# Performance work log

Hardware: AMD Instinct MI355X
Metric: run time of the kernel (lower is better)

Reference implementation:

```python
import jax, jax.numpy as jnp
import numpy as np

NUM_HEADS = 16
KEY_DIM = 64
VALUE_DIM = 64
UPDATE_STEPS_MAX = 3  # loop runs UPDATE_STEPS_MAX+1 attention evaluations, eps=0 so no early exit
LN_EPS = 1e-5


def _layernorm(x, gamma, beta):
    mu = jnp.mean(x, axis=-1, keepdims=True)
    var = jnp.var(x, axis=-1, keepdims=True)
    return (x - mu) * jax.lax.rsqrt(var + LN_EPS) * gamma + beta


def setup_inputs() -> dict:
    key = jax.random.key(0)
    ks = jax.random.split(key, 16)
    B, S, D = 2, 2048, 1024
    Hd = NUM_HEADS * KEY_DIM
    Vd = NUM_HEADS * VALUE_DIM
    s = 1.0 / np.sqrt(D)
    return {
        'query': jax.random.normal(ks[0], (B, S, D), jnp.float32),
        'key':   jax.random.normal(ks[1], (B, S, D), jnp.float32),
        'value': jax.random.normal(ks[2], (B, S, D), jnp.float32),
        'Wq': jax.random.normal(ks[3], (D, Hd), jnp.float32) * s,
        'bq': jnp.zeros((Hd,), jnp.float32),
        'Wk': jax.random.normal(ks[4], (D, Hd), jnp.float32) * s,
        'bk': jnp.zeros((Hd,), jnp.float32),
        'Wv': jax.random.normal(ks[5], (D, Vd), jnp.float32) * s,
        'bv': jnp.zeros((Vd,), jnp.float32),
        'Wo': jax.random.normal(ks[6], (Vd, D), jnp.float32) * s,
        'bo': jnp.zeros((D,), jnp.float32),
        'gamma': jnp.ones((KEY_DIM,), jnp.float32),
        'beta':  jnp.zeros((KEY_DIM,), jnp.float32),
    }


def reference(query, key, value, Wq, bq, Wk, bk, Wv, bv, Wo, bo, gamma, beta):
    B, Sq, D = query.shape
    Sk = key.shape[1]
    # projections -> (B, H, S, d)
    q = (query @ Wq + bq).reshape(B, Sq, NUM_HEADS, KEY_DIM).transpose(0, 2, 1, 3)
    k = (key   @ Wk + bk).reshape(B, Sk, NUM_HEADS, KEY_DIM).transpose(0, 2, 1, 3)
    v = (value @ Wv + bv).reshape(B, Sk, NUM_HEADS, VALUE_DIM).transpose(0, 2, 1, 3)
    # pattern normalization (applied once before the Hopfield loop)
    q = _layernorm(q, gamma, beta)
    k = _layernorm(k, gamma, beta)
    scale = jnp.sqrt(jnp.asarray(KEY_DIM, q.dtype))
    # Hopfield iterations: UPDATE_STEPS_MAX query refinements + final readout
    for i in range(UPDATE_STEPS_MAX + 1):
        scores = jnp.einsum('bhqd,bhkd->bhqk', q, k) / scale
        attn = jax.nn.softmax(scores, axis=-1)
        if i < UPDATE_STEPS_MAX:
            q = jnp.einsum('bhqk,bhkd->bhqd', attn, k)
    out = jnp.einsum('bhqk,bhkd->bhqd', attn, v)  # (B,H,Sq,VALUE_DIM)
    out = out.transpose(0, 2, 1, 3).reshape(B, Sq, NUM_HEADS * VALUE_DIM)
    return out @ Wo + bo
```

## Files before the change

### kernel.cpp

```cpp
#include <hip/hip_runtime.h>

typedef unsigned short u16;
typedef __attribute__((ext_vector_type(8))) short bf16x8;
typedef __attribute__((ext_vector_type(4))) short bf16x4;
typedef __attribute__((ext_vector_type(4))) float f32x4;
typedef __attribute__((ext_vector_type(4))) u16 u16x4;

#define C1 0.18033688011112042f
#define NEGM (-64.0f*C1)

#define GLDS(g, l) __builtin_amdgcn_global_load_lds( \
    (const __attribute__((address_space(1))) void*)(g), \
    (__attribute__((address_space(3))) void*)(l), 16, 0, 0)

__device__ __forceinline__ float fastexp2(float x){
  float r;
  asm("v_exp_f32 %0, %1" : "=v"(r) : "v"(x));
  return r;
}

__device__ __forceinline__ unsigned cvtpk(float x0, float x1){
  unsigned r;
  asm("v_cvt_pk_bf16_f32 %0, %1, %2" : "=v"(r) : "v"(x0), "v"(x1));
  return r;
}

__device__ __forceinline__ bf16x4 pk4(float x0, float x1, float x2, float x3){
  union { unsigned u[2]; bf16x4 b; } o;
  o.u[0] = cvtpk(x0, x1);
  o.u[1] = cvtpk(x2, x3);
  return o.b;
}

__device__ __forceinline__ u16 f2bf(float x){
  unsigned u = __float_as_uint(x);
  u += 0x7fffu + ((u >> 16) & 1u);
  return (u16)(u >> 16);
}
__device__ __forceinline__ float bf2f(u16 h){ return __uint_as_float(((unsigned)h) << 16); }
__device__ __forceinline__ void fsplit(float x, u16 &h, u16 &l){
  h = f2bf(x);
  l = f2bf(x - bf2f(h));
}

__device__ __forceinline__ int swz(int slot, int r){
  return slot ^ (r & 7);
}

__device__ __forceinline__ bf16x8 frag(const bf16x8* lds, int r, int slot){
  return lds[r*8 + swz(slot, r)];
}

__device__ __forceinline__ bf16x4 frag64(const bf16x8* lds, int r, int slot, int half){
  return ((const bf16x4*)&lds[r*8 + swz(slot, r)])[half ^ ((r >> 3) & 1)];
}

template<int ROWS>
__device__ __forceinline__ void stage_glds(bf16x8* lds, const u16* __restrict__ g,
                                           size_t row0, int ldg, int col0, int tid, int w){
#pragma unroll
  for (int p = 0; p < ROWS/32; ++p){
    int idx = p*256 + tid;
    int r = idx >> 3, slot = idx & 7;
    int ss = swz(slot, r);
    GLDS(g + (row0 + (size_t)r)*(size_t)ldg + col0 + ss*8, &lds[p*256 + (w<<6)]);
  }
}

__device__ __forceinline__ f32x4 mfma3(bf16x8 xh, bf16x8 xl, bf16x8 yh, bf16x8 yl, f32x4 c){
  c = __builtin_amdgcn_mfma_f32_16x16x32_bf16(xh, yh, c, 0, 0, 0);
  c = __builtin_amdgcn_mfma_f32_16x16x32_bf16(xh, yl, c, 0, 0, 0);
  c = __builtin_amdgcn_mfma_f32_16x16x32_bf16(xl, yh, c, 0, 0, 0);
  return c;
}

__device__ __forceinline__ void exchange_hi(const f32x4* X, int srcA, int srcB, bool sel_hi,
                                            bf16x8& oh0, bf16x8& oh1)
{
  unsigned hi[8];
#pragma unroll
  for (int a = 0; a < 4; ++a)
#pragma unroll
    for (int b0 = 0; b0 < 2; ++b0)
      hi[a*2+b0] = cvtpk(X[a][2*b0], X[a][2*b0+1]);
  unsigned OH[8];
#pragma unroll
  for (int f = 0; f < 8; ++f){
    const int t0 = (f>>2)*4 + (f&1);
    const int sl = ((f&3)>>1) ? srcB : srcA;
    unsigned h0 = (unsigned)__shfl((int)hi[t0],     sl, 64);
    unsigned h2 = (unsigned)__shfl((int)hi[t0 + 2], sl, 64);
    OH[f] = sel_hi ? h2 : h0;
  }
  union U { unsigned u[4]; bf16x8 b; };
  U a0, a1;
#pragma unroll
  for (int c = 0; c < 4; ++c){ a0.u[c]=OH[c]; a1.u[c]=OH[4+c]; }
  oh0=a0.b; oh1=a1.b;
}

__global__ void __launch_bounds__(256) k_split3(
    const float* __restrict__ xq, const float* __restrict__ xk, const float* __restrict__ xv,
    u16* __restrict__ qh, u16* __restrict__ kh, u16* __restrict__ vh, int n4){
  const int which = blockIdx.y;
  const float* x = which == 0 ? xq : which == 1 ? xk : xv;
  u16* hh = which == 0 ? qh : which == 1 ? kh : vh;
  for (int i = blockIdx.x*256 + threadIdx.x; i < n4; i += gridDim.x*256){
    float4 v = ((const float4*)x)[i];
    u16x4 h;
    h[0] = f2bf(v.x); h[1] = f2bf(v.y); h[2] = f2bf(v.z); h[3] = f2bf(v.w);
    *(u16x4*)(hh + (size_t)i*4) = h;
  }
}

__global__ void __launch_bounds__(256) k_wsplit4(
    const float* __restrict__ W0, const float* __restrict__ W1,
    const float* __restrict__ W2, const float* __restrict__ W3,
    u16* __restrict__ T0h, u16* __restrict__ T1h, u16* __restrict__ T2h,
    u16* __restrict__ T3h, u16* __restrict__ T3l){
  const int which = blockIdx.z;
  const float* W = which == 0 ? W0 : which == 1 ? W1 : which == 2 ? W2 : W3;
  u16* Th = which == 0 ? T0h : which == 1 ? T1h : which == 2 ? T2h : T3h;
  __shared__ float t[32][33];
  int tx = threadIdx.x & 31, ty = threadIdx.x >> 5;
  int n0 = blockIdx.x*32, k0 = blockIdx.y*32;
#pragma unroll
  for (int i = 0; i < 4; ++i)
    t[ty + 8*i][tx] = W[(size_t)(k0 + ty + 8*i)*1024 + n0 + tx];
  __syncthreads();
#pragma unroll
  for (int i = 0; i < 4; ++i){
    int n = n0 + ty + 8*i, k = k0 + tx;
    if (which == 3){
      u16 a, b; fsplit(t[tx][ty + 8*i], a, b);
      Th[(size_t)n*1024 + k] = a;
      T3l[(size_t)n*1024 + k] = b;
    } else {
      Th[(size_t)n*1024 + k] = f2bf(t[tx][ty + 8*i]);
    }
  }
}

template<int MODE, bool SPLIT>
__global__ void __launch_bounds__(256, 3) k_proj(
    const u16* __restrict__ Ah, const u16* __restrict__ Al,
    const u16* __restrict__ Bh, const u16* __restrict__ Bl,
    const float* __restrict__ bias, const float* __restrict__ gamma, const float* __restrict__ beta,
    u16* __restrict__ Nh,
    u16* __restrict__ Th,
    float* __restrict__ Fo)
{
  __shared__ bf16x8 sAh[128*8], sBh[64*8];
  __shared__ bf16x8 sAl[SPLIT ? 128*8 : 1], sBl[SPLIT ? 64*8 : 1];
  const int tid = threadIdx.x, lane = tid & 63, w = tid >> 6;
  const int cl = lane & 15, gq = lane >> 4;
  const int nt = blockIdx.x, mt = blockIdx.y;
  f32x4 acc[2][4] = {};
  for (int kt = 0; kt < 16; ++kt){
    __syncthreads();
    stage_glds<128>(sAh, Ah, (size_t)mt*128, 1024, kt*64, tid, w);
    stage_glds<64>(sBh, Bh, (size_t)nt*64, 1024, kt*64, tid, w);
    if constexpr (SPLIT){
      stage_glds<128>(sAl, Al, (size_t)mt*128, 1024, kt*64, tid, w);
      stage_glds<64>(sBl, Bl, (size_t)nt*64, 1024, kt*64, tid, w);
    }
    __syncthreads();
#pragma unroll
    for (int ks = 0; ks < 2; ++ks){
      const int slot = ks*4 + gq;
      bf16x8 ah0 = frag(sAh, w*32 + cl, slot);
      bf16x8 ah1 = frag(sAh, w*32 + 16 + cl, slot);
      if constexpr (SPLIT){
        bf16x8 al0 = frag(sAl, w*32 + cl, slot);
        bf16x8 al1 = frag(sAl, w*32 + 16 + cl, slot);
#pragma unroll
        for (int f = 0; f < 4; ++f){
          bf16x8 bh_ = frag(sBh, f*16 + cl, slot);
          bf16x8 bl_ = frag(sBl, f*16 + cl, slot);
          acc[0][f] = mfma3(ah0, al0, bh_, bl_, acc[0][f]);
          acc[1][f] = mfma3(ah1, al1, bh_, bl_, acc[1][f]);
        }
      } else {
#pragma unroll
        for (int f = 0; f < 4; ++f){
          bf16x8 bh_ = frag(sBh, f*16 + cl, slot);
          acc[0][f] = __builtin_amdgcn_mfma_f32_16x16x32_bf16(ah0, bh_, acc[0][f], 0, 0, 0);
          acc[1][f] = __builtin_amdgcn_mfma_f32_16x16x32_bf16(ah1, bh_, acc[1][f], 0, 0, 0);
        }
      }
    }
  }
  float bv[4];
#pragma unroll
  for (int f = 0; f < 4; ++f) bv[f] = bias[nt*64 + f*16 + cl];
  float gm[4], bt[4];
  if constexpr (MODE <= 1){
#pragma unroll
    for (int f = 0; f < 4; ++f){ gm[f] = gamma[f*16 + cl]; bt[f] = beta[f*16 + cl]; }
  }
#pragma unroll
  for (int mi = 0; mi < 2; ++mi){
    float v[4][4];
#pragma unroll
    for (int f = 0; f < 4; ++f)
#pragma unroll
      for (int r = 0; r < 4; ++r) v[f][r] = acc[mi][f][r] + bv[f];
    if constexpr (MODE <= 1){
#pragma unroll
      for (int r = 0; r < 4; ++r){
        float s1 = v[0][r] + v[1][r] + v[2][r] + v[3][r];
        float s2 = v[0][r]*v[0][r] + v[1][r]*v[1][r] + v[2][r]*v[2][r] + v[3][r]*v[3][r];
#pragma unroll
        for (int d = 1; d < 16; d <<= 1){ s1 += __shfl_xor(s1, d); s2 += __shfl_xor(s2, d); }
        float mu = s1 * (1.f/64.f);
        float var = s2 * (1.f/64.f) - mu*mu;
        float rs = rsqrtf(var + 1e-5f);
#pragma unroll
        for (int f = 0; f < 4; ++f) v[f][r] = (v[f][r] - mu)*rs*gm[f] + bt[f];
      }
    }
    const int mrow = mt*128 + w*32 + mi*16 + gq*4;
    if constexpr (MODE == 3){
#pragma unroll
      for (int f = 0; f < 4; ++f)
#pragma unroll
        for (int r = 0; r < 4; ++r)
          Fo[(size_t)(mrow + r)*1024 + nt*64 + f*16 + cl] = v[f][r];
    } else {
      const int b = mrow >> 11, srow = mrow & 2047;
      const size_t hb = (size_t)(b*16 + nt);
      if constexpr (MODE <= 1){
#pragma unroll
        for (int f = 0; f < 4; ++f)
#pragma unroll
          for (int r = 0; r < 4; ++r)
            Nh[(hb*2048 + srow + r)*64 + f*16 + cl] = f2bf(v[f][r]);
      }
      if constexpr (MODE == 1 || MODE == 2){
        const int srow_sw = srow ^ (((cl >> 3) & 1) << 2);
#pragma unroll
        for (int f = 0; f < 4; ++f){
          u16x4 h4;
#pragma unroll
          for (int r = 0; r < 4; ++r) h4[r] = f2bf(v[f][r]);
          *(u16x4*)(Th + (hb*64 + f*16 + cl)*2048 + srow_sw) = h4;
        }
      }
    }
  }
}

__global__ void __launch_bounds__(512, 4) k_hopfield(
    const u16* __restrict__ Qh,
    const u16* __restrict__ Kh,
    const u16* __restrict__ Kth,
    const u16* __restrict__ Vth,
    u16* __restrict__ Oh, u16* __restrict__ Ol)
{
  __shared__ bf16x8 sKh[2][512], sTh[2][512];
  const int tid = threadIdx.x, lane = tid & 63, w = tid >> 6;
  const int cl = lane & 15, gq = lane >> 4;
  int flat = blockIdx.x;
  flat = (flat & 7)*64 + (flat >> 3);
  const int bh = flat >> 4, qt = flat & 15;
  const size_t base = (size_t)bh * (2048*64);
  const int q = qt*128 + w*16 + cl;

  const int sr = tid >> 3, ss = swz(tid & 7, sr);
  const size_t offK = base + (size_t)sr*64 + ss*8;
  const size_t offT = base + (size_t)sr*2048 + ss*8;
  const int wslot = w << 6;

  bf16x8 qfh[2];
#pragma unroll
  for (int ks = 0; ks < 2; ++ks)
    qfh[ks] = *(const bf16x8*)(Qh + base + (size_t)q*64 + ks*32 + gq*8);

  const int srcA = cl + ((gq & 1) << 5);
  const int srcB = srcA + 16;
  const bool sel_hi = gq >= 2;

  const bf16x4 ones = {(short)0x3F80, (short)0x3F80, (short)0x3F80, (short)0x3F80};
  f32x4 accL = {0,0,0,0};
  f32x4 accO[4] = {};

  GLDS(Kh  + offK, &sKh[0][wslot]);
  GLDS(Kth + offT, &sTh[0][wslot]);
  __syncthreads();

#pragma unroll 2
  for (int t = 0; t < 128; ++t){
    const int cur = t & 1, kt = t & 31;
    if (t < 127){
      const int nt_ = t + 1, nb = nt_ & 1, nit = nt_ >> 5, nkt = nt_ & 31;
      const u16* th = (nit < 3) ? Kth : Vth;
      GLDS(Kh + offK + (size_t)nkt*4096, &sKh[nb][wslot]);
      GLDS(th + offT + (size_t)nkt*64,   &sTh[nb][wslot]);
    }
    f32x4 S[4] = {};
    __builtin_amdgcn_s_setprio(1);
#pragma unroll
    for (int ks = 0; ks < 2; ++ks){
      const int slot = ks*4 + gq;
#pragma unroll
      for (int i = 0; i < 4; ++i){
        bf16x8 kh_ = frag(&sKh[cur][0], i*16 + cl, slot);
        S[i] = __builtin_amdgcn_mfma_f32_16x16x32_bf16(kh_, qfh[ks], S[i], 0, 0, 0);
      }
    }
    __builtin_amdgcn_s_setprio(0);
#pragma unroll
    for (int i = 0; i < 4; ++i)
#pragma unroll
      for (int r = 0; r < 4; ++r)
        S[i][r] = fastexp2(__builtin_fmaf(S[i][r], C1, NEGM));
    bf16x4 pf[4];
#pragma unroll
    for (int a = 0; a < 4; ++a)
      pf[a] = pk4(S[a][0], S[a][1], S[a][2], S[a][3]);
    __builtin_amdgcn_s_setprio(1);
#pragma unroll
    for (int a = 0; a < 4; ++a)
      accL = __builtin_amdgcn_mfma_f32_16x16x16bf16_1k(ones, pf[a], accL, 0, 0, 0);
#pragma unroll
    for (int db = 0; db < 4; ++db)
#pragma unroll
      for (int a = 0; a < 4; ++a){
        bf16x4 vh_ = frag64(&sTh[cur][0], db*16 + cl, 2*a + (gq>>1), gq&1);
        accO[db] = __builtin_amdgcn_mfma_f32_16x16x16bf16_1k(vh_, pf[a], accO[db], 0, 0, 0);
      }
    __builtin_amdgcn_s_setprio(0);
    if (kt == 31){
      const float inv = 1.f / accL[0];
      f32x4 vals[4];
#pragma unroll
      for (int db = 0; db < 4; ++db)
#pragma unroll
        for (int r = 0; r < 4; ++r) vals[db][r] = accO[db][r]*inv;
      if (t < 127){
        exchange_hi(vals, srcA, srcB, sel_hi, qfh[0], qfh[1]);
        accL = f32x4{0,0,0,0};
#pragma unroll
        for (int db = 0; db < 4; ++db) accO[db] = f32x4{0,0,0,0};
      } else {
        const int b = bh >> 4, h = bh & 15;
        const size_t row = (size_t)b*2048 + q;
#pragma unroll
        for (int db = 0; db < 4; ++db){
          u16x4 h4, l4;
#pragma unroll
          for (int r = 0; r < 4; ++r){ u16 a_, b_; fsplit(vals[db][r], a_, b_); h4[r] = a_; l4[r] = b_; }
          size_t ix = row*1024 + h*64 + db*16 + gq*4;
          *(u16x4*)(Oh + ix) = h4;
          *(u16x4*)(Ol + ix) = l4;
        }
      }
    }
    __syncthreads();
  }
}

extern "C" void kernel_launch(void* const* d_in, const int* in_sizes, int n_in,
                              void* d_out, int out_size, void* d_ws, size_t ws_size,
                              hipStream_t stream) {
  (void)in_sizes; (void)n_in; (void)out_size; (void)ws_size;
  const float* query = (const float*)d_in[0];
  const float* key   = (const float*)d_in[1];
  const float* value = (const float*)d_in[2];
  const float* Wq = (const float*)d_in[3];
  const float* bq = (const float*)d_in[4];
  const float* Wk = (const float*)d_in[5];
  const float* bk = (const float*)d_in[6];
  const float* Wv = (const float*)d_in[7];
  const float* bv = (const float*)d_in[8];
  const float* Wo = (const float*)d_in[9];
  const float* bo = (const float*)d_in[10];
  const float* gamma = (const float*)d_in[11];
  const float* beta  = (const float*)d_in[12];
  float* out = (float*)d_out;

  char* ws = (char*)d_ws;
  const size_t MB = 1024*1024;
  u16* inq_h = (u16*)(ws + 0*MB),  *inq_l = (u16*)(ws + 8*MB);
  u16* ink_h = (u16*)(ws + 16*MB);
  u16* inv_h = (u16*)(ws + 32*MB);
  u16* wq_h = (u16*)(ws + 48*MB);
  u16* wk_h = (u16*)(ws + 52*MB);
  u16* wv_h = (u16*)(ws + 56*MB);
  u16* wo_h = (u16*)(ws + 60*MB), *wo_l = (u16*)(ws + 62*MB);
  u16* Qh  = (u16*)(ws + 64*MB);
  u16* Kh  = (u16*)(ws + 80*MB);
  u16* Kth = (u16*)(ws + 96*MB);
  u16* Vth = (u16*)(ws + 112*MB);
  u16* Oh = inq_h, *Ol = inq_l;

  const int n4 = 4096*1024/4;
  k_split3<<<dim3(1024, 3), dim3(256), 0, stream>>>(query, key, value,
                                                    inq_h, ink_h, inv_h, n4);
  k_wsplit4<<<dim3(32,32,4), dim3(256), 0, stream>>>(Wq, Wk, Wv, Wo,
                                                     wq_h, wk_h, wv_h, wo_h, wo_l);

  k_proj<0,false><<<dim3(16,32), dim3(256), 0, stream>>>(inq_h, nullptr, wq_h, nullptr, bq, gamma, beta,
                                                         Qh, nullptr, nullptr);
  k_proj<1,false><<<dim3(16,32), dim3(256), 0, stream>>>(ink_h, nullptr, wk_h, nullptr, bk, gamma, beta,
                                                         Kh, Kth, nullptr);
  k_proj<2,false><<<dim3(16,32), dim3(256), 0, stream>>>(inv_h, nullptr, wv_h, nullptr, bv, nullptr, nullptr,
                                                         nullptr, Vth, nullptr);

  k_hopfield<<<dim3(512), dim3(512), 0, stream>>>(Qh, Kh, Kth, Vth, Oh, Ol);

  k_proj<3,true><<<dim3(16,32), dim3(256), 0, stream>>>(Oh, Ol, wo_h, wo_l, bo, nullptr, nullptr,
                                                        nullptr, nullptr, out);
}
```

Measured before the change: 281.1 us.

## Process two query groups per wave in Hopfield kernel to reuse K/V fragments

The Hopfield attention kernel drops from 512 to 256 threads per block, and each wave now handles 32 queries as two 16-row groups instead of 16. Each K and V fragment read from LDS feeds two MFMAs, which halves LDS fragment traffic per MFMA. Each thread issues two async global-to-LDS loads per tile to fill the same buffers. Register pressure roughly doubles for the accumulators and occupancy falls (launch bounds 256,2), which may expose latency.

After: 286.9 us. 1.02x slower.

```diff
diff --git a/kernel.cpp b/kernel.cpp
--- a/kernel.cpp
+++ b/kernel.cpp
@@ -250,7 +250,7 @@
   }
 }
 
-__global__ void __launch_bounds__(512, 4) k_hopfield(
+__global__ void __launch_bounds__(256, 2) k_hopfield(
     const u16* __restrict__ Qh,
     const u16* __restrict__ Kh,
     const u16* __restrict__ Kth,
@@ -264,28 +264,33 @@
   flat = (flat & 7)*64 + (flat >> 3);
   const int bh = flat >> 4, qt = flat & 15;
   const size_t base = (size_t)bh * (2048*64);
-  const int q = qt*128 + w*16 + cl;
 
   const int sr = tid >> 3, ss = swz(tid & 7, sr);
   const size_t offK = base + (size_t)sr*64 + ss*8;
   const size_t offT = base + (size_t)sr*2048 + ss*8;
   const int wslot = w << 6;
 
-  bf16x8 qfh[2];
-#pragma unroll
-  for (int ks = 0; ks < 2; ++ks)
-    qfh[ks] = *(const bf16x8*)(Qh + base + (size_t)q*64 + ks*32 + gq*8);
+  bf16x8 qfh[2][2];
+#pragma unroll
+  for (int qg = 0; qg < 2; ++qg){
+    const int q = qt*128 + w*32 + qg*16 + cl;
+#pragma unroll
+    for (int ks = 0; ks < 2; ++ks)
+      qfh[qg][ks] = *(const bf16x8*)(Qh + base + (size_t)q*64 + ks*32 + gq*8);
+  }
 
   const int srcA = cl + ((gq & 1) << 5);
   const int srcB = srcA + 16;
   const bool sel_hi = gq >= 2;
 
   const bf16x4 ones = {(short)0x3F80, (short)0x3F80, (short)0x3F80, (short)0x3F80};
-  f32x4 accL = {0,0,0,0};
-  f32x4 accO[4] = {};
-
-  GLDS(Kh  + offK, &sKh[0][wslot]);
-  GLDS(Kth + offT, &sTh[0][wslot]);
+  f32x4 accL[2] = {};
+  f32x4 accO[2][4] = {};
+
+  GLDS(Kh  + offK,        &sKh[0][wslot]);
+  GLDS(Kh  + offK + 2048, &sKh[0][wslot + 256]);
+  GLDS(Kth + offT,         &sTh[0][wslot]);
+  GLDS(Kth + offT + 65536, &sTh[0][wslot + 256]);
   __syncthreads();
 
 #pragma unroll 2
@@ -294,10 +299,14 @@
     if (t < 127){
       const int nt_ = t + 1, nb = nt_ & 1, nit = nt_ >> 5, nkt = nt_ & 31;
       const u16* th = (nit < 3) ? Kth : Vth;
-      GLDS(Kh + offK + (size_t)nkt*4096, &sKh[nb][wslot]);
-      GLDS(th + offT + (size_t)nkt*64,   &sTh[nb][wslot]);
-    }
-    f32x4 S[4] = {};
+      const size_t oK = offK + (size_t)nkt*4096;
+      const size_t oT = offT + (size_t)nkt*64;
+      GLDS(Kh + oK,        &sKh[nb][wslot]);
+      GLDS(Kh + oK + 2048, &sKh[nb][wslot + 256]);
+      GLDS(th + oT,         &sTh[nb][wslot]);
+      GLDS(th + oT + 65536, &sTh[nb][wslot + 256]);
+    }
+    f32x4 S[2][4] = {};
     __builtin_amdgcn_s_setprio(1);
 #pragma unroll
     for (int ks = 0; ks < 2; ++ks){
@@ -305,54 +314,65 @@
 #pragma unroll
       for (int i = 0; i < 4; ++i){
         bf16x8 kh_ = frag(&sKh[cur][0], i*16 + cl, slot);
-        S[i] = __builtin_amdgcn_mfma_f32_16x16x32_bf16(kh_, qfh[ks], S[i], 0, 0, 0);
+        S[0][i] = __builtin_amdgcn_mfma_f32_16x16x32_bf16(kh_, qfh[0][ks], S[0][i], 0, 0, 0);
+        S[1][i] = __builtin_amdgcn_mfma_f32_16x16x32_bf16(kh_, qfh[1][ks], S[1][i], 0, 0, 0);
       }
     }
     __builtin_amdgcn_s_setprio(0);
-#pragma unroll
-    for (int i = 0; i < 4; ++i)
-#pragma unroll
-      for (int r = 0; r < 4; ++r)
-        S[i][r] = fastexp2(__builtin_fmaf(S[i][r], C1, NEGM));
-    bf16x4 pf[4];
-#pragma unroll
-    for (int a = 0; a < 4; ++a)
-      pf[a] = pk4(S[a][0], S[a][1], S[a][2], S[a][3]);
+    bf16x4 pf[2][4];
+#pragma unroll
+    for (int qg = 0; qg < 2; ++qg){
+#pragma unroll
+      for (int i = 0; i < 4; ++i)
+#pragma unroll
+        for (int r = 0; r < 4; ++r)
+          S[qg][i][r] = fastexp2(__builtin_fmaf(S[qg][i][r], C1, NEGM));
+#pragma unroll
+      for (int a = 0; a < 4; ++a)
+        pf[qg][a] = pk4(S[qg][a][0], S[qg][a][1], S[qg][a][2], S[qg][a][3]);
+    }
     __builtin_amdgcn_s_setprio(1);
 #pragma unroll
-    for (int a = 0; a < 4; ++a)
-      accL = __builtin_amdgcn_mfma_f32_16x16x16bf16_1k(ones, pf[a], accL, 0, 0, 0);
+    for (int a = 0; a < 4; ++a){
+      accL[0] = __builtin_amdgcn_mfma_f32_16x16x16bf16_1k(ones, pf[0][a], accL[0], 0, 0, 0);
+      accL[1] = __builtin_amdgcn_mfma_f32_16x16x16bf16_1k(ones, pf[1][a], accL[1], 0, 0, 0);
+    }
 #pragma unroll
     for (int db = 0; db < 4; ++db)
 #pragma unroll
       for (int a = 0; a < 4; ++a){
         bf16x4 vh_ = frag64(&sTh[cur][0], db*16 + cl, 2*a + (gq>>1), gq&1);
-        accO[db] = __builtin_amdgcn_mfma_f32_16x16x16bf16_1k(vh_, pf[a], accO[db], 0, 0, 0);
+        accO[0][db] = __builtin_amdgcn_mfma_f32_16x16x16bf16_1k(vh_, pf[0][a], accO[0][db], 0, 0, 0);
+        accO[1][db] = __builtin_amdgcn_mfma_f32_16x16x16bf16_1k(vh_, pf[1][a], accO[1][db], 0, 0, 0);
       }
     __builtin_amdgcn_s_setprio(0);
     if (kt == 31){
-      const float inv = 1.f / accL[0];
-      f32x4 vals[4];
-#pragma unroll
-      for (int db = 0; db < 4; ++db)
-#pragma unroll
-        for (int r = 0; r < 4; ++r) vals[db][r] = accO[db][r]*inv;
-      if (t < 127){
-        exchange_hi(vals, srcA, srcB, sel_hi, qfh[0], qfh[1]);
-        accL = f32x4{0,0,0,0};
-#pragma unroll
-        for (int db = 0; db < 4; ++db) accO[db] = f32x4{0,0,0,0};
-      } else {
-        const int b = bh >> 4, h = bh & 15;
-        const size_t row = (size_t)b*2048 + q;
-#pragma unroll
-        for (int db = 0; db < 4; ++db){
-          u16x4 h4, l4;
-#pragma unroll
-          for (int r = 0; r < 4; ++r){ u16 a_, b_; fsplit(vals[db][r], a_, b_); h4[r] = a_; l4[r] = b_; }
-          size_t ix = row*1024 + h*64 + db*16 + gq*4;
-          *(u16x4*)(Oh + ix) = h4;
-          *(u16x4*)(Ol + ix) = l4;
+#pragma unroll
+      for (int qg = 0; qg < 2; ++qg){
+        const float inv = 1.f / accL[qg][0];
+        f32x4 vals[4];
+#pragma unroll
+        for (int db = 0; db < 4; ++db)
+#pragma unroll
+          for (int r = 0; r < 4; ++r) vals[db][r] = accO[qg][db][r]*inv;
+        if (t < 127){
+          exchange_hi(vals, srcA, srcB, sel_hi, qfh[qg][0], qfh[qg][1]);
+          accL[qg] = f32x4{0,0,0,0};
+#pragma unroll
+          for (int db = 0; db < 4; ++db) accO[qg][db] = f32x4{0,0,0,0};
+        } else {
+          const int b = bh >> 4, h = bh & 15;
+          const int q = qt*128 + w*32 + qg*16 + cl;
+          const size_t row = (size_t)b*2048 + q;
+#pragma unroll
+          for (int db = 0; db < 4; ++db){
+            u16x4 h4, l4;
+#pragma unroll
+            for (int r = 0; r < 4; ++r){ u16 a_, b_; fsplit(vals[db][r], a_, b_); h4[r] = a_; l4[r] = b_; }
+            size_t ix = row*1024 + h*64 + db*16 + gq*4;
+            *(u16x4*)(Oh + ix) = h4;
+            *(u16x4*)(Ol + ix) = l4;
+          }
         }
       }
     }
@@ -407,7 +427,7 @@
   k_proj<2,false><<<dim3(16,32), dim3(256), 0, stream>>>(inv_h, nullptr, wv_h, nullptr, bv, nullptr, nullptr,
                                                          nullptr, Vth, nullptr);
 
-  k_hopfield<<<dim3(512), dim3(512), 0, stream>>>(Qh, Kh, Kth, Vth, Oh, Ol);
+  k_hopfield<<<dim3(512), dim3(256), 0, stream>>>(Qh, Kh, Kth, Vth, Oh, Ol);
 
   k_proj<3,true><<<dim3(16,32), dim3(256), 0, stream>>>(Oh, Ol, wo_h, wo_l, bo, nullptr, nullptr,
                                                         nullptr, nullptr, out);
```
